# Kernel tuning notes

Measured on AMD Instinct MI355X. Metric: run time of the kernel, lower is better.

Reference implementation:

```python
import jax, jax.numpy as jnp
import numpy as np

SUPPORT = 1
NEIGHBOR = 20
STRIDE = 2
BS, V = 4, 2048


def _gather(feat, idx):
    # feat: (b, v, c), idx: (b, v, n) -> (b, v, n, c)
    b = feat.shape[0]
    return feat[jnp.arange(b)[:, None, None], idx]


def get_neighbor_index(vertices, k):
    # pairwise squared distances, take k nearest excluding self
    inner = jnp.einsum('bid,bjd->bij', vertices, vertices)
    sq = jnp.sum(vertices * vertices, axis=-1)
    dist = sq[:, :, None] - 2.0 * inner + sq[:, None, :]
    _, idx = jax.lax.top_k(-dist, k + 1)
    return idx[:, :, 1:]


def conv_layer(w, b, d, nbr, vertices, fmap, out_c):
    bs, v, n = nbr.shape
    diff = _gather(vertices, nbr) - vertices[:, :, None, :]  # (b,v,n,3)
    diff = diff / jnp.maximum(jnp.linalg.norm(diff, axis=-1, keepdims=True), 1e-12)
    dirn = d / jnp.maximum(jnp.linalg.norm(d, axis=0, keepdims=True), 1e-12)
    theta = jnp.einsum('bvnd,de->bvne', diff, dirn)  # (b,v,n,S*out)
    feat = fmap @ w + b  # (b,v,(S+1)*out)
    center = feat[..., :out_c]
    support = _gather(feat[..., out_c:], nbr)  # (b,v,n,S*out)
    act = (theta * support).reshape(bs, v, n, SUPPORT, out_c)
    act = jnp.sum(jnp.max(act, axis=2), axis=2)  # max over neighbors, sum over supports
    return center + act


LAYERS = [('c0', 3, 32), ('c1', 32, 64), ('c12', 64, 64), ('c13', 64, 64), ('c14', 64, 64),
          ('p1', 64, 64), ('c2', 64, 128), ('c3', 128, 256), ('c4', 256, 1024),
          ('c42', 1024, 1024), ('c43', 1024, 1024), ('c44', 1024, 1024)]


def _layer_params(key, in_c, out_c):
    k1, k2, k3 = jax.random.split(key, 3)
    stdv = 1.0 / np.sqrt((SUPPORT + 1) * out_c)
    w = jax.random.uniform(k1, (in_c, (SUPPORT + 1) * out_c), minval=-stdv, maxval=stdv, dtype=jnp.float32)
    b = jax.random.uniform(k2, ((SUPPORT + 1) * out_c,), minval=-stdv, maxval=stdv, dtype=jnp.float32)
    d = jax.random.uniform(k3, (3, SUPPORT * out_c), minval=-stdv, maxval=stdv, dtype=jnp.float32)
    return w, b, d


def setup_inputs() -> dict:
    key = jax.random.key(0)
    keys = jax.random.split(key, 20)
    inp = {'vertices': jax.random.normal(keys[0], (BS, V, 3), dtype=jnp.float32)}
    for i, (name, ic, oc) in enumerate(LAYERS):
        w, b, d = _layer_params(keys[i + 1], ic, oc)
        inp[name + '_w'], inp[name + '_b'], inp[name + '_d'] = w, b, d
    inp['fc1_w'] = jax.random.normal(keys[14], (1024, 256), dtype=jnp.float32) * 0.02
    inp['fc1_b'] = jnp.zeros((256,), jnp.float32)
    inp['bn_g'] = jnp.ones((256,), jnp.float32)
    inp['bn_b'] = jnp.zeros((256,), jnp.float32)
    inp['fc2_w'] = jax.random.normal(keys[15], (256, 40), dtype=jnp.float32) * 0.02
    inp['fc2_b'] = jnp.zeros((40,), jnp.float32)
    return inp


def reference(vertices, c0_w, c0_b, c0_d, c1_w, c1_b, c1_d, c12_w, c12_b, c12_d, c13_w, c13_b, c13_d, c14_w, c14_b, c14_d, p1_w, p1_b, p1_d, c2_w, c2_b, c2_d, c3_w, c3_b, c3_d, c4_w, c4_b, c4_d, c42_w, c42_b, c42_d, c43_w, c43_b, c43_d, c44_w, c44_b, c44_d, fc1_w, fc1_b, bn_g, bn_b, fc2_w, fc2_b):
    nbr = get_neighbor_index(vertices, NEIGHBOR)
    fm = conv_layer(c0_w, c0_b, c0_d, nbr, vertices, vertices, 32)
    fm = conv_layer(c1_w, c1_b, c1_d, nbr, vertices, fm, 64)
    fm = conv_layer(c12_w, c12_b, c12_d, nbr, vertices, fm, 64)
    fm = conv_layer(c13_w, c13_b, c13_d, nbr, vertices, fm, 64)
    fm = conv_layer(c14_w, c14_b, c14_d, nbr, vertices, fm, 64)
    # pool_1: conv, neighbor-max pooling, stride-2 vertex subsampling
    fm = conv_layer(p1_w, p1_b, p1_d, nbr, vertices, fm, 64)
    fm = jnp.max(_gather(fm, nbr), axis=2)
    sub = jnp.arange(0, vertices.shape[1], STRIDE)
    vertices2 = vertices[:, sub]
    fm = fm[:, sub]
    nbr2 = get_neighbor_index(vertices2, NEIGHBOR)
    fm = conv_layer(c2_w, c2_b, c2_d, nbr2, vertices2, fm, 128)
    fm = conv_layer(c3_w, c3_b, c3_d, nbr2, vertices2, fm, 256)
    fm = conv_layer(c4_w, c4_b, c4_d, nbr2, vertices2, fm, 1024)
    fm = conv_layer(c42_w, c42_b, c42_d, nbr2, vertices2, fm, 1024)
    fm = conv_layer(c43_w, c43_b, c43_d, nbr2, vertices2, fm, 1024)
    fm = conv_layer(c44_w, c44_b, c44_d, nbr2, vertices2, fm, 1024)
    g = jnp.max(fm, axis=1)  # (b, 1024) global max pool
    h = g @ fc1_w + fc1_b  # dropout = identity in eval
    h = h * jax.lax.rsqrt(jnp.float32(1.0 + 1e-5)) * bn_g + bn_b  # BN eval, running mean 0 / var 1
    h = jax.nn.relu(h)
    return h @ fc2_w + fc2_b
```

## Files before the change

### kernel.cpp

```cpp
#include <hip/hip_runtime.h>
#include <float.h>
#include <math.h>

#define BS 4
#define V1 2048
#define V2 1024
#define NB 20
#define KSEL 21

typedef __attribute__((ext_vector_type(8))) short short8v;
typedef __attribute__((ext_vector_type(4))) float f32x4;

__device__ __forceinline__ unsigned short f2bf(float x) {
    union { float f; unsigned u; } v; v.f = x;
    unsigned r = (v.u + 0x7fffu + ((v.u >> 16) & 1u)) >> 16;
    return (unsigned short)r;
}
__device__ __forceinline__ float bf2f(unsigned short h) {
    return __uint_as_float((unsigned)h << 16);
}
__device__ __forceinline__ unsigned umin32(unsigned a, unsigned b) { return a < b ? a : b; }

__device__ __forceinline__ void gload16(const void* g, void* l) {
    __builtin_amdgcn_global_load_lds((const __attribute__((address_space(1))) void*)g,
                                     (__attribute__((address_space(3))) void*)l, 16, 0, 0);
}

template<int SLOTS>
__global__ __launch_bounds__(256)
void knn_wave_kernel(const float* __restrict__ verts, int stride, int* __restrict__ nbr,
                     float* __restrict__ diffn)
{
    constexpr int Vv = SLOTS * 64;
    __shared__ float xs[Vv], ys[Vv], zs[Vv];
    int tid = threadIdx.x;
    int lane = tid & 63;
    int wv = tid >> 6;
    int b = blockIdx.x / (Vv / 4);
    int q0 = (blockIdx.x % (Vv / 4)) * 4;
    const float* vb = verts + (size_t)b * V1 * 3;
    for (int p = tid; p < Vv; p += 256) {
        xs[p] = vb[(size_t)p * stride * 3 + 0];
        ys[p] = vb[(size_t)p * stride * 3 + 1];
        zs[p] = vb[(size_t)p * stride * 3 + 2];
    }
    __syncthreads();
    int i = q0 + wv;
    float xi = xs[i], yi = ys[i], zi = zs[i];
    float sqi = xi * xi + yi * yi + zi * zi;
    unsigned keys[SLOTS];
    #pragma unroll
    for (int s = 0; s < SLOTS; ++s) {
        int j = s * 64 + lane;
        float xj = xs[j], yj = ys[j], zj = zs[j];
        float sqj = xj * xj + yj * yj + zj * zj;
        float d = sqi - 2.0f * (xi * xj + yi * yj + zi * zj) + sqj;
        unsigned u = __float_as_uint(d);
        u = (u & 0x80000000u) ? ~u : (u | 0x80000000u);
        keys[s] = (u & ~31u) | (unsigned)s;
    }
    const unsigned UMAX = 0xFFFFFFFFu;
    unsigned c0 = UMAX, c1 = UMAX, c2 = UMAX, c3 = UMAX;
    #pragma unroll
    for (int s = 0; s < SLOTS; ++s) c0 = umin32(c0, keys[s]);
    #pragma unroll
    for (int s = 0; s < SLOTS; ++s) { unsigned k = keys[s]; if (k > c0) c1 = umin32(c1, k); }
    #pragma unroll
    for (int s = 0; s < SLOTS; ++s) { unsigned k = keys[s]; if (k > c1) c2 = umin32(c2, k); }
    #pragma unroll
    for (int s = 0; s < SLOTS; ++s) { unsigned k = keys[s]; if (k > c2) c3 = umin32(c3, k); }

    unsigned lm = c0;
    int myj = 0;
    for (int it = 0; it < KSEL; ++it) {
        unsigned m = lm;
        #pragma unroll
        for (int off = 1; off < 64; off <<= 1)
            m = umin32(m, (unsigned)__shfl_xor((int)m, off));
        unsigned long long bal = __ballot(lm == m);
        int wl = __ffsll(bal) - 1;
        int slot = (int)(m & 31u);
        int j = slot * 64 + wl;
        if (lane == it - 1) myj = j;
        if (lane == wl) {
            c0 = c1; c1 = c2; c2 = c3; c3 = UMAX;
            if (c0 == UMAX) {
                #pragma unroll
                for (int s = 0; s < SLOTS; ++s) {
                    unsigned k = keys[s];
                    if (k > m) c0 = umin32(c0, k);
                }
            }
            lm = c0;
        }
    }
    if (lane < NB) {
        nbr[((size_t)b * Vv + i) * NB + lane] = myj;
        float dx = xs[myj] - xi, dy = ys[myj] - yi, dz = zs[myj] - zi;
        float nrm = sqrtf(dx * dx + dy * dy + dz * dz);
        float inv = 1.0f / fmaxf(nrm, 1e-12f);
        float* dout = diffn + (((size_t)b * Vv + i) * NB + lane) * 3;
        dout[0] = dx * inv; dout[1] = dy * inv; dout[2] = dz * inv;
    }
}

struct ConvTArgs {
    const float* W[11];
    unsigned short* Wt[11];
    int K[11];
    int N[11];
    int tileoff[12];
};

__global__ __launch_bounds__(256)
void convT_all(ConvTArgs a)
{
    __shared__ float t[32][33];
    int g = blockIdx.x;
    int L = 0;
    #pragma unroll
    for (int q = 0; q < 10; ++q) if (g >= a.tileoff[q + 1]) L = q + 1;
    int rel = g - a.tileoff[L];
    int K = a.K[L], N = a.N[L];
    int tilesN = N >> 5;
    int k0 = (rel / tilesN) << 5, n0 = (rel % tilesN) << 5;
    const float* W = a.W[L];
    unsigned short* Wt = a.Wt[L];
    int tx = threadIdx.x & 31, ty = threadIdx.x >> 5;
    #pragma unroll
    for (int r = ty; r < 32; r += 8) t[r][tx] = W[(size_t)(k0 + r) * N + n0 + tx];
    __syncthreads();
    #pragma unroll
    for (int r = ty; r < 32; r += 8) Wt[(size_t)(n0 + r) * K + k0 + tx] = f2bf(t[tx][r]);
}

__global__ __launch_bounds__(256)
void c0_kernel(const float* __restrict__ verts, const float* __restrict__ W,
               const float* __restrict__ Bv, unsigned short* __restrict__ feat)
{
    int t = blockIdx.x * 256 + threadIdx.x;
    if (t >= BS * V1 * 64) return;
    int n = t & 63, m = t >> 6;
    float x = verts[(size_t)m * 3 + 0];
    float y = verts[(size_t)m * 3 + 1];
    float z = verts[(size_t)m * 3 + 2];
    feat[t] = f2bf(x * W[n] + y * W[64 + n] + z * W[128 + n] + Bv[n]);
}

template<int BK, int BM, int BN>
__global__ __launch_bounds__(256)
void gemm_mfma(const unsigned short* __restrict__ A, const unsigned short* __restrict__ Wt,
               const float* __restrict__ bias, unsigned short* __restrict__ C,
               int M, int N, int K)
{
    constexpr int RB = BK * 2;
    constexpr int TA = BM * RB;
    constexpr int TB = BN * RB;
    constexpr int SWM = (BK == 64) ? 7 : 3;
    constexpr int FI = BM / 32, FJ = BN / 32;
    constexpr int RA = TA / 4096, RBN = TB / 4096;
    constexpr int RMAX = (RA > RBN) ? RA : RBN;
    __shared__ __align__(16) char smem[TA + TB];
    int tid = threadIdx.x;
    int lane = tid & 63, wid = tid >> 6;
    int wr = wid >> 1, wc = wid & 1;

    int nwg = gridDim.x * gridDim.y;
    int orig = blockIdx.y * gridDim.x + blockIdx.x;
    int wg = orig;
    if ((nwg & 7) == 0) wg = (orig & 7) * (nwg >> 3) + (orig >> 3);
    int m0 = (wg / gridDim.x) * BM;
    int n0 = (wg % gridDim.x) * BN;

    f32x4 acc[FI][FJ] = {};

    int srow[RMAX], soffe[RMAX];
    #pragma unroll
    for (int r = 0; r < RMAX; ++r) {
        int L = r * 4096 + tid * 16;
        int row = L / RB;
        int off = (L % RB) ^ ((row & SWM) << 4);
        srow[r] = row; soffe[r] = off >> 1;
    }

    for (int kt = 0; kt < K; kt += BK) {
        #pragma unroll
        for (int r = 0; r < RA; ++r)
            gload16(A + (size_t)(m0 + srow[r]) * K + kt + soffe[r],
                    smem + r * 4096 + wid * 1024);
        #pragma unroll
        for (int r = 0; r < RBN; ++r)
            gload16(Wt + (size_t)(n0 + srow[r]) * K + kt + soffe[r],
                    smem + TA + r * 4096 + wid * 1024);
        asm volatile("s_waitcnt vmcnt(0)" ::: "memory");
        __syncthreads();
        #pragma unroll
        for (int ks = 0; ks < BK / 32; ++ks) {
            short8v av[FI], bv[FJ];
            #pragma unroll
            for (int i = 0; i < FI; ++i) {
                int row = wr * (BM / 2) + i * 16 + (lane & 15);
                int off = (ks * 64 + ((lane >> 4) * 16)) ^ ((row & SWM) << 4);
                av[i] = *(const short8v*)(smem + row * RB + off);
            }
            #pragma unroll
            for (int j = 0; j < FJ; ++j) {
                int row = wc * (BN / 2) + j * 16 + (lane & 15);
                int off = (ks * 64 + ((lane >> 4) * 16)) ^ ((row & SWM) << 4);
                bv[j] = *(const short8v*)(smem + TA + row * RB + off);
            }
            #pragma unroll
            for (int i = 0; i < FI; ++i)
                #pragma unroll
                for (int j = 0; j < FJ; ++j)
                    acc[i][j] = __builtin_amdgcn_mfma_f32_16x16x32_bf16(av[i], bv[j], acc[i][j], 0, 0, 0);
        }
        __syncthreads();
    }
    #pragma unroll
    for (int i = 0; i < FI; ++i) {
        #pragma unroll
        for (int j = 0; j < FJ; ++j) {
            int col = n0 + wc * (BN / 2) + j * 16 + (lane & 15);
            int rowb = m0 + wr * (BM / 2) + i * 16 + ((lane >> 4) * 4);
            float bv2 = bias[col];
            #pragma unroll
            for (int v = 0; v < 4; ++v)
                C[(size_t)(rowb + v) * N + col] = f2bf(acc[i][j][v] + bv2);
        }
    }
}

__global__ __launch_bounds__(256)
void act_kernel(const unsigned short* __restrict__ feat, const int* __restrict__ nbr,
                const float* __restrict__ diffn, const float* __restrict__ dmat,
                unsigned short* __restrict__ outh, int Vv, int OC)
{
    int OC4 = OC >> 2;
    int t = blockIdx.x * 256 + threadIdx.x;
    int total = BS * Vv * OC4;
    if (t >= total) return;
    int c4 = t % OC4;
    int v = (t / OC4) % Vv;
    int b = t / (OC4 * Vv);
    const float4* d4 = (const float4*)dmat;
    float4 D0 = d4[c4], D1 = d4[OC4 + c4], D2 = d4[2 * OC4 + c4];
    float n0 = sqrtf(D0.x * D0.x + D1.x * D1.x + D2.x * D2.x);
    float n1 = sqrtf(D0.y * D0.y + D1.y * D1.y + D2.y * D2.y);
    float n2 = sqrtf(D0.z * D0.z + D1.z * D1.z + D2.z * D2.z);
    float n3 = sqrtf(D0.w * D0.w + D1.w * D1.w + D2.w * D2.w);
    float i0 = 1.0f / fmaxf(n0, 1e-12f);
    float i1 = 1.0f / fmaxf(n1, 1e-12f);
    float i2 = 1.0f / fmaxf(n2, 1e-12f);
    float i3 = 1.0f / fmaxf(n3, 1e-12f);
    D0.x *= i0; D0.y *= i1; D0.z *= i2; D0.w *= i3;
    D1.x *= i0; D1.y *= i1; D1.z *= i2; D1.w *= i3;
    D2.x *= i0; D2.y *= i1; D2.z *= i2; D2.w *= i3;

    const int* nb = nbr + ((size_t)b * Vv + v) * NB;
    const float* dfn = diffn + ((size_t)b * Vv + v) * NB * 3;
    const ushort4* frow = (const ushort4*)feat;
    size_t rowstride = (size_t)(2 * OC4);
    const ushort4* fsup = frow + (size_t)b * Vv * rowstride + OC4 + c4;
    float4 m = make_float4(-FLT_MAX, -FLT_MAX, -FLT_MAX, -FLT_MAX);
    for (int n = 0; n < NB; ++n) {
        int idx = nb[n];
        float e0 = dfn[3 * n + 0], e1 = dfn[3 * n + 1], e2 = dfn[3 * n + 2];
        ushort4 s = fsup[(size_t)idx * rowstride];
        float th;
        th = e0 * D0.x + e1 * D1.x + e2 * D2.x; m.x = fmaxf(m.x, th * bf2f(s.x));
        th = e0 * D0.y + e1 * D1.y + e2 * D2.y; m.y = fmaxf(m.y, th * bf2f(s.y));
        th = e0 * D0.z + e1 * D1.z + e2 * D2.z; m.z = fmaxf(m.z, th * bf2f(s.z));
        th = e0 * D0.w + e1 * D1.w + e2 * D2.w; m.w = fmaxf(m.w, th * bf2f(s.w));
    }
    ushort4 cen = frow[(size_t)b * Vv * rowstride + (size_t)v * rowstride + c4];
    size_t oidx = ((size_t)b * Vv + v) * OC4 + c4;
    ushort4 h;
    h.x = f2bf(bf2f(cen.x) + m.x); h.y = f2bf(bf2f(cen.y) + m.y);
    h.z = f2bf(bf2f(cen.z) + m.z); h.w = f2bf(bf2f(cen.w) + m.w);
    ((ushort4*)outh)[oidx] = h;
}

__global__ __launch_bounds__(256)
void act1024_kernel(const unsigned short* __restrict__ feat, const int* __restrict__ nbr,
                    const float* __restrict__ diffn, const float* __restrict__ dmat,
                    unsigned short* __restrict__ outh)
{
    const int OC4 = 256;
    int g = blockIdx.x;
    int b = (g & 7) >> 1;
    int v = ((g >> 3) << 1) | (g & 1);
    int c4 = threadIdx.x;
    const float4* d4 = (const float4*)dmat;
    float4 D0 = d4[c4], D1 = d4[OC4 + c4], D2 = d4[2 * OC4 + c4];
    float n0 = sqrtf(D0.x * D0.x + D1.x * D1.x + D2.x * D2.x);
    float n1 = sqrtf(D0.y * D0.y + D1.y * D1.y + D2.y * D2.y);
    float n2 = sqrtf(D0.z * D0.z + D1.z * D1.z + D2.z * D2.z);
    float n3 = sqrtf(D0.w * D0.w + D1.w * D1.w + D2.w * D2.w);
    float i0 = 1.0f / fmaxf(n0, 1e-12f);
    float i1 = 1.0f / fmaxf(n1, 1e-12f);
    float i2 = 1.0f / fmaxf(n2, 1e-12f);
    float i3 = 1.0f / fmaxf(n3, 1e-12f);
    D0.x *= i0; D0.y *= i1; D0.z *= i2; D0.w *= i3;
    D1.x *= i0; D1.y *= i1; D1.z *= i2; D1.w *= i3;
    D2.x *= i0; D2.y *= i1; D2.z *= i2; D2.w *= i3;

    const int* nb = nbr + ((size_t)b * V2 + v) * NB;
    const float* dfn = diffn + ((size_t)b * V2 + v) * NB * 3;
    const ushort4* frow = (const ushort4*)feat;
    const size_t rowstride = 2 * OC4;
    const ushort4* fsup = frow + (size_t)b * V2 * rowstride + OC4 + c4;
    float4 m = make_float4(-FLT_MAX, -FLT_MAX, -FLT_MAX, -FLT_MAX);
    for (int n = 0; n < NB; ++n) {
        int idx = nb[n];
        float e0 = dfn[3 * n + 0], e1 = dfn[3 * n + 1], e2 = dfn[3 * n + 2];
        ushort4 s = fsup[(size_t)idx * rowstride];
        float th;
        th = e0 * D0.x + e1 * D1.x + e2 * D2.x; m.x = fmaxf(m.x, th * bf2f(s.x));
        th = e0 * D0.y + e1 * D1.y + e2 * D2.y; m.y = fmaxf(m.y, th * bf2f(s.y));
        th = e0 * D0.z + e1 * D1.z + e2 * D2.z; m.z = fmaxf(m.z, th * bf2f(s.z));
        th = e0 * D0.w + e1 * D1.w + e2 * D2.w; m.w = fmaxf(m.w, th * bf2f(s.w));
    }
    ushort4 cen = frow[((size_t)b * V2 + v) * rowstride + c4];
    size_t oidx = ((size_t)b * V2 + v) * OC4 + c4;
    ushort4 h;
    h.x = f2bf(bf2f(cen.x) + m.x); h.y = f2bf(bf2f(cen.y) + m.y);
    h.z = f2bf(bf2f(cen.z) + m.z); h.w = f2bf(bf2f(cen.w) + m.w);
    ((ushort4*)outh)[oidx] = h;
}

__global__ __launch_bounds__(256)
void pool_kernel(const ushort4* __restrict__ fmh, const int* __restrict__ nbr,
                 ushort4* __restrict__ outp)
{
    const int C4 = 16;
    int t = blockIdx.x * 256 + threadIdx.x;
    int total = BS * V2 * C4;
    if (t >= total) return;
    int c = t % C4;
    int v2 = (t / C4) % V2;
    int b = t / (C4 * V2);
    const int* nb = nbr + ((size_t)b * V1 + 2 * v2) * NB;
    float4 m = make_float4(-FLT_MAX, -FLT_MAX, -FLT_MAX, -FLT_MAX);
    for (int n = 0; n < NB; ++n) {
        int idx = nb[n];
        ushort4 s = fmh[((size_t)b * V1 + idx) * C4 + c];
        m.x = fmaxf(m.x, bf2f(s.x)); m.y = fmaxf(m.y, bf2f(s.y));
        m.z = fmaxf(m.z, bf2f(s.z)); m.w = fmaxf(m.w, bf2f(s.w));
    }
    ushort4 h;
    h.x = f2bf(m.x); h.y = f2bf(m.y); h.z = f2bf(m.z); h.w = f2bf(m.w);
    outp[((size_t)b * V2 + v2) * C4 + c] = h;
}

__global__ __launch_bounds__(256)
void gmax_part(const unsigned short* __restrict__ fm, float* __restrict__ part)
{
    int c = blockIdx.x * 256 + threadIdx.x;
    int ch = blockIdx.y;
    int b = blockIdx.z;
    float m = -FLT_MAX;
    for (int v = ch * 128; v < (ch + 1) * 128; ++v)
        m = fmaxf(m, bf2f(fm[((size_t)b * V2 + v) * 1024 + c]));
    part[((size_t)b * 8 + ch) * 1024 + c] = m;
}

__global__ __launch_bounds__(256)
void fc1_part(const float* __restrict__ gpart, const float* __restrict__ fc1w,
              float* __restrict__ hpart)
{
    int b = blockIdx.x, kg = blockIdx.y;
    int j = threadIdx.x;
    __shared__ float gs[128];
    if (j < 128) {
        float m = -FLT_MAX;
        #pragma unroll
        for (int ch = 0; ch < 8; ++ch)
            m = fmaxf(m, gpart[((size_t)b * 8 + ch) * 1024 + kg * 128 + j]);
        gs[j] = m;
    }
    __syncthreads();
    float h = 0.0f;
    #pragma unroll 4
    for (int k = 0; k < 128; ++k)
        h = fmaf(gs[k], fc1w[(size_t)(kg * 128 + k) * 256 + j], h);
    hpart[((size_t)b * 8 + kg) * 256 + j] = h;
}

__global__ __launch_bounds__(256)
void head2_kernel(const float* __restrict__ hpart, const float* __restrict__ fc1b,
                  const float* __restrict__ bng, const float* __restrict__ bnb,
                  const float* __restrict__ fc2w, const float* __restrict__ fc2b,
                  float* __restrict__ outp)
{
    __shared__ float hs[256];
    __shared__ float part[4][40];
    int b = blockIdx.x;
    int j = threadIdx.x;
    float s = fc1b[j];
    #pragma unroll
    for (int kg = 0; kg < 8; ++kg) s += hpart[((size_t)b * 8 + kg) * 256 + j];
    const float rc = 0.99999500003749937f;
    s = s * rc * bng[j] + bnb[j];
    hs[j] = fmaxf(s, 0.0f);
    __syncthreads();
    int ks = j >> 6, jo = j & 63;
    if (jo < 40) {
        float o = 0.0f;
        for (int k = ks * 64; k < ks * 64 + 64; ++k)
            o = fmaf(hs[k], fc2w[(size_t)k * 40 + jo], o);
        part[ks][jo] = o;
    }
    __syncthreads();
    if (j < 40)
        outp[(size_t)b * 40 + j] = fc2b[j] + part[0][j] + part[1][j] + part[2][j] + part[3][j];
}

extern "C" void kernel_launch(void* const* d_in, const int* in_sizes, int n_in,
                              void* d_out, int out_size, void* d_ws, size_t ws_size,
                              hipStream_t stream)
{
    (void)in_sizes; (void)n_in; (void)out_size; (void)ws_size;
    const float* verts = (const float*)d_in[0];
    auto Wp = [&](int i) { return (const float*)d_in[1 + 3 * i]; };
    auto Bp = [&](int i) { return (const float*)d_in[2 + 3 * i]; };
    auto Dp = [&](int i) { return (const float*)d_in[3 + 3 * i]; };
    const float* fc1w = (const float*)d_in[37];
    const float* fc1b = (const float*)d_in[38];
    const float* bng  = (const float*)d_in[39];
    const float* bnb  = (const float*)d_in[40];
    const float* fc2w = (const float*)d_in[41];
    const float* fc2b = (const float*)d_in[42];

    static const int IC[12] = {3, 32, 64, 64, 64, 64, 64, 128, 256, 1024, 1024, 1024};
    static const int OC[12] = {32, 64, 64, 64, 64, 64, 128, 256, 1024, 1024, 1024, 1024};

    char* ws = (char*)d_ws;
    size_t off = 0;
    auto alloc = [&](size_t bytes) {
        void* p = ws + off;
        off += (bytes + 255) & ~(size_t)255;
        return p;
    };
    int*   nbr1   = (int*)alloc((size_t)BS * V1 * NB * 4);
    int*   nbr2   = (int*)alloc((size_t)BS * V2 * NB * 4);
    float* diffn1 = (float*)alloc((size_t)BS * V1 * NB * 3 * 4);
    float* diffn2 = (float*)alloc((size_t)BS * V2 * NB * 3 * 4);
    unsigned short* feat = (unsigned short*)alloc((size_t)BS * V2 * 2048 * 2);
    unsigned short* fmh0 = (unsigned short*)alloc((size_t)BS * V2 * 1024 * 2);
    unsigned short* fmh1 = (unsigned short*)alloc((size_t)BS * V2 * 1024 * 2);
    float* gpart  = (float*)alloc((size_t)BS * 8 * 1024 * 4);
    float* hpart  = (float*)alloc((size_t)BS * 8 * 256 * 4);

    unsigned short* WtBuf[12];
    {
        size_t total = 0;
        for (int i = 1; i < 12; ++i) total += (size_t)(2 * OC[i]) * IC[i];
        unsigned short* base = (unsigned short*)alloc(total * 2);
        size_t o2 = 0;
        for (int i = 1; i < 12; ++i) { WtBuf[i] = base + o2; o2 += (size_t)(2 * OC[i]) * IC[i]; }
    }
    {
        ConvTArgs a;
        int toff = 0;
        for (int i = 1; i < 12; ++i) {
            int K = IC[i], N = 2 * OC[i];
            a.W[i - 1] = Wp(i);
            a.Wt[i - 1] = WtBuf[i];
            a.K[i - 1] = K;
            a.N[i - 1] = N;
            a.tileoff[i - 1] = toff;
            toff += (K / 32) * (N / 32);
        }
        a.tileoff[11] = toff;
        convT_all<<<toff, 256, 0, stream>>>(a);
    }

    auto gemm = [&](const unsigned short* A, int li, unsigned short* Cc, int M) {
        int K = IC[li], N = 2 * OC[li];
        if (N >= 1024) {
            dim3 gdim(N / 128, M / 128);
            gemm_mfma<64, 128, 128><<<gdim, 256, 0, stream>>>(A, WtBuf[li], Bp(li), Cc, M, N, K);
        } else if (K % 64 == 0) {
            dim3 gdim(N / 64, M / 64);
            gemm_mfma<64, 64, 64><<<gdim, 256, 0, stream>>>(A, WtBuf[li], Bp(li), Cc, M, N, K);
        } else {
            dim3 gdim(N / 64, M / 64);
            gemm_mfma<32, 64, 64><<<gdim, 256, 0, stream>>>(A, WtBuf[li], Bp(li), Cc, M, N, K);
        }
    };
    auto act = [&](const unsigned short* f, const int* nbr, const float* dfn, const float* d,
                   unsigned short* outh, int Vv, int oc) {
        if (oc == 1024) {
            act1024_kernel<<<BS * V2, 256, 0, stream>>>(f, nbr, dfn, d, outh);
        } else {
            int total = BS * Vv * (oc / 4);
            act_kernel<<<(total + 255) / 256, 256, 0, stream>>>(f, nbr, dfn, d, outh, Vv, oc);
        }
    };

    knn_wave_kernel<32><<<BS * V1 / 4, 256, 0, stream>>>(verts, 1, nbr1, diffn1);
    knn_wave_kernel<16><<<BS * V2 / 4, 256, 0, stream>>>(verts, 2, nbr2, diffn2);

    c0_kernel<<<(BS * V1 * 64 + 255) / 256, 256, 0, stream>>>(verts, Wp(0), Bp(0), feat);
    unsigned short* hb[2] = {fmh0, fmh1};
    int pb = 0;
    act(feat, nbr1, diffn1, Dp(0), hb[pb], V1, OC[0]);
    const unsigned short* cur = hb[pb]; pb ^= 1;

    for (int i = 1; i < 6; ++i) {
        gemm(cur, i, feat, BS * V1);
        act(feat, nbr1, diffn1, Dp(i), hb[pb], V1, OC[i]);
        cur = hb[pb]; pb ^= 1;
    }

    {
        int total = BS * V2 * 16;
        pool_kernel<<<(total + 255) / 256, 256, 0, stream>>>(
            (const ushort4*)cur, nbr1, (ushort4*)hb[pb]);
        cur = hb[pb]; pb ^= 1;
    }

    for (int i = 6; i < 12; ++i) {
        gemm(cur, i, feat, BS * V2);
        act(feat, nbr2, diffn2, Dp(i), hb[pb], V2, OC[i]);
        cur = hb[pb]; pb ^= 1;
    }

    gmax_part<<<dim3(4, 8, BS), 256, 0, stream>>>(cur, gpart);
    fc1_part<<<dim3(BS, 8), 256, 0, stream>>>(gpart, fc1w, hpart);
    head2_kernel<<<BS, 256, 0, stream>>>(hpart, fc1b, bng, bnb, fc2w, fc2b, (float*)d_out);
}
```

Before: 516.3 us.

## Merge both kNN launches into one kernel and fuse c0 linear with its activation

The two kNN kernels (full and stride-2 vertex sets) now run as one launch, with blocks split between the two problems by index and sharing one shared-memory buffer sized for the larger set. The c0 feature kernel and the first activation kernel are replaced by act0_kernel. It computes the 3-input linear layer for the center and for each neighbor on the fly from vertex coordinates, does the direction dot product and the neighbor max, and writes bf16 output. This removes two launches and the feat intermediate round trip, at the cost of recomputing neighbor support features (cheap at in_c=3) and a larger static LDS footprint for the smaller kNN blocks.

```diff
diff --git a/kernel.cpp b/kernel.cpp
--- a/kernel.cpp
+++ b/kernel.cpp
@@ -27,18 +27,18 @@
 }
 
 template<int SLOTS>
-__global__ __launch_bounds__(256)
-void knn_wave_kernel(const float* __restrict__ verts, int stride, int* __restrict__ nbr,
-                     float* __restrict__ diffn)
+__device__ __forceinline__ void knn_body(const float* __restrict__ vb, int stride,
+                                         int* __restrict__ nbr, float* __restrict__ diffn,
+                                         float* smem, int rel)
 {
     constexpr int Vv = SLOTS * 64;
-    __shared__ float xs[Vv], ys[Vv], zs[Vv];
+    float* xs = smem;
+    float* ys = smem + Vv;
+    float* zs = smem + 2 * Vv;
     int tid = threadIdx.x;
     int lane = tid & 63;
     int wv = tid >> 6;
-    int b = blockIdx.x / (Vv / 4);
-    int q0 = (blockIdx.x % (Vv / 4)) * 4;
-    const float* vb = verts + (size_t)b * V1 * 3;
+    int q0 = rel * 4;
     for (int p = tid; p < Vv; p += 256) {
         xs[p] = vb[(size_t)p * stride * 3 + 0];
         ys[p] = vb[(size_t)p * stride * 3 + 1];
@@ -95,12 +95,33 @@
         }
     }
     if (lane < NB) {
-        nbr[((size_t)b * Vv + i) * NB + lane] = myj;
+        nbr[(size_t)i * NB + lane] = myj;
         float dx = xs[myj] - xi, dy = ys[myj] - yi, dz = zs[myj] - zi;
         float nrm = sqrtf(dx * dx + dy * dy + dz * dz);
         float inv = 1.0f / fmaxf(nrm, 1e-12f);
-        float* dout = diffn + (((size_t)b * Vv + i) * NB + lane) * 3;
+        float* dout = diffn + ((size_t)i * NB + lane) * 3;
         dout[0] = dx * inv; dout[1] = dy * inv; dout[2] = dz * inv;
+    }
+}
+
+__global__ __launch_bounds__(256)
+void knn_all_kernel(const float* __restrict__ verts,
+                    int* __restrict__ nbr1, float* __restrict__ diffn1,
+                    int* __restrict__ nbr2, float* __restrict__ diffn2)
+{
+    __shared__ float smem[3 * V1];
+    int g = blockIdx.x;
+    if (g < BS * V1 / 4) {
+        int b = g / (V1 / 4), rel = g % (V1 / 4);
+        knn_body<32>(verts + (size_t)b * V1 * 3, 1,
+                     nbr1 + (size_t)b * V1 * NB, diffn1 + (size_t)b * V1 * NB * 3,
+                     smem, rel);
+    } else {
+        int g2 = g - BS * V1 / 4;
+        int b = g2 / (V2 / 4), rel = g2 % (V2 / 4);
+        knn_body<16>(verts + (size_t)b * V1 * 3, 2,
+                     nbr2 + (size_t)b * V2 * NB, diffn2 + (size_t)b * V2 * NB * 3,
+                     smem, rel);
     }
 }
 
@@ -135,16 +156,66 @@
 }
 
 __global__ __launch_bounds__(256)
-void c0_kernel(const float* __restrict__ verts, const float* __restrict__ W,
-               const float* __restrict__ Bv, unsigned short* __restrict__ feat)
+void act0_kernel(const float* __restrict__ verts, const float* __restrict__ W,
+                 const float* __restrict__ Bv, const float* __restrict__ dmat,
+                 const int* __restrict__ nbr, const float* __restrict__ diffn,
+                 unsigned short* __restrict__ outh)
 {
     int t = blockIdx.x * 256 + threadIdx.x;
-    if (t >= BS * V1 * 64) return;
-    int n = t & 63, m = t >> 6;
-    float x = verts[(size_t)m * 3 + 0];
-    float y = verts[(size_t)m * 3 + 1];
-    float z = verts[(size_t)m * 3 + 2];
-    feat[t] = f2bf(x * W[n] + y * W[64 + n] + z * W[128 + n] + Bv[n]);
+    int c4 = t & 7;
+    int v = (t >> 3) & (V1 - 1);
+    int b = t >> 14;
+    const float4* d4 = (const float4*)dmat;
+    float4 D0 = d4[c4], D1 = d4[8 + c4], D2 = d4[16 + c4];
+    float n0 = sqrtf(D0.x * D0.x + D1.x * D1.x + D2.x * D2.x);
+    float n1 = sqrtf(D0.y * D0.y + D1.y * D1.y + D2.y * D2.y);
+    float n2 = sqrtf(D0.z * D0.z + D1.z * D1.z + D2.z * D2.z);
+    float n3 = sqrtf(D0.w * D0.w + D1.w * D1.w + D2.w * D2.w);
+    float i0 = 1.0f / fmaxf(n0, 1e-12f);
+    float i1 = 1.0f / fmaxf(n1, 1e-12f);
+    float i2 = 1.0f / fmaxf(n2, 1e-12f);
+    float i3 = 1.0f / fmaxf(n3, 1e-12f);
+    D0.x *= i0; D0.y *= i1; D0.z *= i2; D0.w *= i3;
+    D1.x *= i0; D1.y *= i1; D1.z *= i2; D1.w *= i3;
+    D2.x *= i0; D2.y *= i1; D2.z *= i2; D2.w *= i3;
+    float dA[4] = {D0.x, D0.y, D0.z, D0.w};
+    float dB[4] = {D1.x, D1.y, D1.z, D1.w};
+    float dC[4] = {D2.x, D2.y, D2.z, D2.w};
+
+    float wcx[4], wcy[4], wcz[4], wsx[4], wsy[4], wsz[4], bc[4], bs[4];
+    #pragma unroll
+    for (int j = 0; j < 4; ++j) {
+        int cc = c4 * 4 + j;
+        wcx[j] = W[cc];       wcy[j] = W[64 + cc];       wcz[j] = W[128 + cc];
+        wsx[j] = W[32 + cc];  wsy[j] = W[96 + cc];       wsz[j] = W[160 + cc];
+        bc[j] = Bv[cc];       bs[j] = Bv[32 + cc];
+    }
+    const float* vb = verts + (size_t)b * V1 * 3;
+    float xv = vb[(size_t)v * 3 + 0];
+    float yv = vb[(size_t)v * 3 + 1];
+    float zv = vb[(size_t)v * 3 + 2];
+    const int* nb_ = nbr + ((size_t)b * V1 + v) * NB;
+    const float* dfn = diffn + ((size_t)b * V1 + v) * NB * 3;
+    float m[4] = {-FLT_MAX, -FLT_MAX, -FLT_MAX, -FLT_MAX};
+    for (int n = 0; n < NB; ++n) {
+        int idx = nb_[n];
+        float e0 = dfn[3 * n + 0], e1 = dfn[3 * n + 1], e2 = dfn[3 * n + 2];
+        float xn = vb[(size_t)idx * 3 + 0];
+        float yn = vb[(size_t)idx * 3 + 1];
+        float zn = vb[(size_t)idx * 3 + 2];
+        #pragma unroll
+        for (int j = 0; j < 4; ++j) {
+            float sup = xn * wsx[j] + yn * wsy[j] + zn * wsz[j] + bs[j];
+            float th = e0 * dA[j] + e1 * dB[j] + e2 * dC[j];
+            m[j] = fmaxf(m[j], th * sup);
+        }
+    }
+    ushort4 h;
+    h.x = f2bf(xv * wcx[0] + yv * wcy[0] + zv * wcz[0] + bc[0] + m[0]);
+    h.y = f2bf(xv * wcx[1] + yv * wcy[1] + zv * wcz[1] + bc[1] + m[1]);
+    h.z = f2bf(xv * wcx[2] + yv * wcy[2] + zv * wcz[2] + bc[2] + m[2]);
+    h.w = f2bf(xv * wcx[3] + yv * wcy[3] + zv * wcz[3] + bc[3] + m[3]);
+    ((ushort4*)outh)[((size_t)b * V1 + v) * 8 + c4] = h;
 }
 
 template<int BK, int BM, int BN>
@@ -499,13 +570,13 @@
         }
     };
 
-    knn_wave_kernel<32><<<BS * V1 / 4, 256, 0, stream>>>(verts, 1, nbr1, diffn1);
-    knn_wave_kernel<16><<<BS * V2 / 4, 256, 0, stream>>>(verts, 2, nbr2, diffn2);
-
-    c0_kernel<<<(BS * V1 * 64 + 255) / 256, 256, 0, stream>>>(verts, Wp(0), Bp(0), feat);
+    knn_all_kernel<<<BS * V1 / 4 + BS * V2 / 4, 256, 0, stream>>>(
+        verts, nbr1, diffn1, nbr2, diffn2);
+
     unsigned short* hb[2] = {fmh0, fmh1};
     int pb = 0;
-    act(feat, nbr1, diffn1, Dp(0), hb[pb], V1, OC[0]);
+    act0_kernel<<<BS * V1 * 8 / 256, 256, 0, stream>>>(
+        verts, Wp(0), Bp(0), Dp(0), nbr1, diffn1, hb[pb]);
     const unsigned short* cur = hb[pb]; pb ^= 1;
 
     for (int i = 1; i < 6; ++i) {
```

Measured after the change: 506.7 us. No clear change (-1.9%).
